# Kernel tuning notes

Measured on AMD Instinct MI355X. Metric: run time of the kernel, lower is better.

The kernel has to match this reference:

```python
import jax, jax.numpy as jnp
import numpy as np

EPS = 1e-12  # matches torch F.normalize default eps in spectral_norm


def _l2norm(v):
    return v / jnp.maximum(jnp.linalg.norm(v), EPS)


def _spectral_norm(W, u):
    # One power-iteration step (torch spectral_norm training behavior).
    # u, v are treated as constants w.r.t. gradients.
    v = jax.lax.stop_gradient(_l2norm(W.T @ u))
    u2 = jax.lax.stop_gradient(_l2norm(W @ v))
    sigma = jnp.einsum('o,oi,i->', u2, W, v)
    return W / sigma


def setup_inputs() -> dict:
    key = jax.random.key(0)
    ks = jax.random.split(key, 8)
    B, C, N = 8, 512, 2048
    d = C // 8
    return {
        'x':  jax.random.normal(ks[0], (B, C, N), dtype=jnp.float32),
        'Wq': jax.random.normal(ks[1], (d, C), dtype=jnp.float32) * (1.0 / np.sqrt(C)),
        'Wk': jax.random.normal(ks[2], (d, C), dtype=jnp.float32) * (1.0 / np.sqrt(C)),
        'Wv': jax.random.normal(ks[3], (C, C), dtype=jnp.float32) * (1.0 / np.sqrt(C)),
        'uq': jax.random.normal(ks[4], (d,), dtype=jnp.float32),
        'uk': jax.random.normal(ks[5], (d,), dtype=jnp.float32),
        'uv': jax.random.normal(ks[6], (C,), dtype=jnp.float32),
        'gamma': jax.random.normal(ks[7], (1,), dtype=jnp.float32) * 0.1,
    }


def reference(x, Wq, Wk, Wv, uq, uk, uv, gamma):
    # x: [B, C, N]
    f = jnp.einsum('oi,bin->bon', _spectral_norm(Wq, uq), x)  # [B, C/8, N]
    g = jnp.einsum('oi,bin->bon', _spectral_norm(Wk, uk), x)  # [B, C/8, N]
    h = jnp.einsum('oi,bin->bon', _spectral_norm(Wv, uv), x)  # [B, C, N]
    scores = jnp.einsum('bdn,bdm->bnm', f, g)                 # f^T g: [B, N, N]
    beta = jax.nn.softmax(scores, axis=1)                      # softmax over dim=1
    o = gamma[0] * jnp.einsum('bcn,bnm->bcm', h, beta) + x    # [B, C, N]
    return o
```

## Files before the change

kernel.cpp:

```cpp
#include <hip/hip_runtime.h>
#include <hip/hip_bf16.h>
#include <math.h>

#define B_ 8
#define C_ 512
#define N_ 2048
#define D_ 64
#define O_ 640

typedef __bf16 bf16x8 __attribute__((ext_vector_type(8)));
typedef float f32x4 __attribute__((ext_vector_type(4)));
typedef unsigned short ushort8_t __attribute__((ext_vector_type(8)));
typedef unsigned short ushort4_t __attribute__((ext_vector_type(4)));

__device__ __forceinline__ unsigned short f2bf(float f) {
    unsigned int u = __builtin_bit_cast(unsigned int, f);
    u += 0x7fffu + ((u >> 16) & 1u);
    return (unsigned short)(u >> 16);
}

__device__ __forceinline__ float fastexp(float x) {
    return exp2f(x * 1.44269504088896340736f);
}

union FragU { ushort8_t u; bf16x8 b; };

__device__ __forceinline__ bf16x8 ldfrag(const unsigned short* p) {
    FragU t; t.u = *(const ushort8_t*)p; return t.b;
}

__device__ __forceinline__ void gload_lds16(const unsigned short* g, unsigned short* l) {
    __builtin_amdgcn_global_load_lds((const __attribute__((address_space(1))) void*)g,
                                     (__attribute__((address_space(3))) void*)l,
                                     16, 0, 0);
}

__global__ __launch_bounds__(512) void k_colvec(const float* __restrict__ Wq,
                                                const float* __restrict__ Wk,
                                                const float* __restrict__ Wv,
                                                const float* __restrict__ uq,
                                                const float* __restrict__ uk,
                                                const float* __restrict__ uv,
                                                float* __restrict__ tpart) {
    int which = blockIdx.y, oq = blockIdx.x;
    const float* W; const float* u; int R;
    if (which == 0)      { W = Wq; u = uq; R = 64;  }
    else if (which == 1) { W = Wk; u = uk; R = 64;  }
    else                 { W = Wv; u = uv; R = 512; }
    int chunk = R >> 2;
    int i = threadIdx.x;
    float s = 0.f;
    int o0 = oq * chunk, o1 = o0 + chunk;
    for (int o = o0; o < o1; ++o) s += W[(size_t)o * 512 + i] * u[o];
    tpart[((which << 2) + oq) * 512 + i] = s;
}

__global__ __launch_bounds__(512) void k_trow(const float* __restrict__ tpart,
                                              float* __restrict__ tvec,
                                              float* __restrict__ t2) {
    int which = blockIdx.x, i = threadIdx.x;
    const float* tp = tpart + (which << 2) * 512;
    float s = tp[i] + tp[512 + i] + tp[1024 + i] + tp[1536 + i];
    tvec[which * 512 + i] = s;
    __shared__ float red[512];
    red[i] = s * s; __syncthreads();
    for (int st = 256; st > 0; st >>= 1) { if (i < st) red[i] += red[i + st]; __syncthreads(); }
    if (i == 0) t2[which] = red[0];
}

__global__ __launch_bounds__(256) void k_rowvec(const float* __restrict__ Wq,
                                                const float* __restrict__ Wk,
                                                const float* __restrict__ Wv,
                                                const float* __restrict__ tvec,
                                                float* __restrict__ wpart) {
    int which = blockIdx.y;
    const float* W; int R;
    if (which == 0)      { W = Wq; R = 64;  }
    else if (which == 1) { W = Wk; R = 64;  }
    else                 { W = Wv; R = 512; }
    int tid = threadIdx.x, lane = tid & 63, wv = tid >> 6;
    int row = blockIdx.x * 4 + wv;
    float ps = 0.f;
    if (row < R) {
        const float4* wr_ = (const float4*)(W + (size_t)row * 512);
        const float4* tv = (const float4*)(tvec + which * 512);
        float4 a0 = wr_[lane * 2], a1 = wr_[lane * 2 + 1];
        float4 b0 = tv[lane * 2], b1 = tv[lane * 2 + 1];
        float s = a0.x * b0.x + a0.y * b0.y + a0.z * b0.z + a0.w * b0.w
                + a1.x * b1.x + a1.y * b1.y + a1.z * b1.z + a1.w * b1.w;
        #pragma unroll
        for (int off = 1; off < 64; off <<= 1) s += __shfl_xor(s, off, 64);
        ps = s * s;
    }
    __shared__ float red[4];
    if (lane == 0) red[wv] = ps;
    __syncthreads();
    if (tid == 0) wpart[which * 128 + blockIdx.x] = red[0] + red[1] + red[2] + red[3];
}

__global__ __launch_bounds__(128) void k_scale(const float* __restrict__ wpart,
                                               const float* __restrict__ t2,
                                               float* __restrict__ scales) {
    int which = blockIdx.x, tid = threadIdx.x;
    float s = wpart[which * 128 + tid];
    #pragma unroll
    for (int off = 1; off < 64; off <<= 1) s += __shfl_xor(s, off, 64);
    __shared__ float r2[2];
    if ((tid & 63) == 0) r2[tid >> 6] = s;
    __syncthreads();
    if (tid == 0) scales[which] = sqrtf(t2[which] / fmaxf(r2[0] + r2[1], 1e-24f));
}

__global__ __launch_bounds__(256) void k_wconv(const float* __restrict__ Wq,
                                               const float* __restrict__ Wk,
                                               const float* __restrict__ Wv,
                                               const float* __restrict__ scales,
                                               unsigned short* __restrict__ Wb) {
    int gid = blockIdx.x * 256 + threadIdx.x;
    int e0 = gid * 8;
    int o = e0 >> 9, i = e0 & 511;
    const float* src; float sc;
    if (o < 64)       { src = Wq + (size_t)o * 512;         sc = scales[0]; }
    else if (o < 128) { src = Wk + (size_t)(o - 64) * 512;  sc = scales[1]; }
    else              { src = Wv + (size_t)(o - 128) * 512; sc = scales[2]; }
    float4 v0 = *(const float4*)(src + i), v1 = *(const float4*)(src + i + 4);
    ushort8_t u;
    u[0] = f2bf(v0.x * sc); u[1] = f2bf(v0.y * sc); u[2] = f2bf(v0.z * sc); u[3] = f2bf(v0.w * sc);
    u[4] = f2bf(v1.x * sc); u[5] = f2bf(v1.y * sc); u[6] = f2bf(v1.z * sc); u[7] = f2bf(v1.w * sc);
    *(ushort8_t*)&Wb[(size_t)o * 512 + i] = u;
}

__global__ __launch_bounds__(256) void k_transpose(const float* __restrict__ x,
                                                   unsigned short* __restrict__ xT) {
    __shared__ float tile[64][33];
    int b = blockIdx.z;
    int n0 = blockIdx.x * 32, c0 = blockIdx.y * 64;
    int tx = threadIdx.x, ty = threadIdx.y;
    #pragma unroll
    for (int k = 0; k < 8; ++k) {
        int c = ty + k * 8;
        tile[c][tx] = x[((size_t)b * C_ + c0 + c) * N_ + n0 + tx];
    }
    __syncthreads();
    #pragma unroll
    for (int k = 0; k < 4; ++k) {
        int n = ty + k * 8;
        unsigned int p = (unsigned int)f2bf(tile[tx * 2][n]) |
                         ((unsigned int)f2bf(tile[tx * 2 + 1][n]) << 16);
        *(unsigned int*)&xT[((size_t)b * N_ + n0 + n) * C_ + c0 + tx * 2] = p;
    }
}

__global__ __launch_bounds__(256) void k_proj(const unsigned short* __restrict__ xT,
                                              const unsigned short* __restrict__ Wb,
                                              unsigned short* __restrict__ fT,
                                              unsigned short* __restrict__ gT,
                                              unsigned short* __restrict__ hb) {
    int b = blockIdx.z, n0 = blockIdx.y * 128, o0 = blockIdx.x * 128;
    int tid = threadIdx.x, lane = tid & 63, w = tid >> 6;
    int wr = w >> 1, wc = w & 1;
    __shared__ __align__(16) unsigned short Sh[16384];
    unsigned short* As = Sh;
    unsigned short* Bs = Sh + 8192;
    f32x4 zero = {0.f, 0.f, 0.f, 0.f};
    f32x4 acc[4][4];
    #pragma unroll
    for (int i = 0; i < 4; ++i)
        #pragma unroll
        for (int j = 0; j < 4; ++j) acc[i][j] = zero;
    int r8 = lane >> 3, s = lane & 7;
    int scol = (s ^ r8) * 8;

    for (int kt = 0; kt < 8; ++kt) {
        #pragma unroll
        for (int q = 0; q < 4; ++q) {
            int chunk = w * 4 + q;
            int row = chunk * 8 + r8;
            gload_lds16(xT + ((size_t)b * N_ + n0 + row) * C_ + kt * 64 + scol, &As[chunk * 512]);
            gload_lds16(Wb + (size_t)(o0 + row) * C_ + kt * 64 + scol, &Bs[chunk * 512]);
        }
        __syncthreads();
        int kg = lane >> 4, r16 = lane & 15;
        #pragma unroll
        for (int kk = 0; kk < 2; ++kk) {
            int sw = kk * 4 + kg;
            bf16x8 af[4];
            #pragma unroll
            for (int i = 0; i < 4; ++i) {
                int row = wr * 64 + i * 16 + r16;
                af[i] = ldfrag(&As[row * 64 + (sw ^ (row & 7)) * 8]);
            }
            #pragma unroll
            for (int j = 0; j < 4; ++j) {
                int row = wc * 64 + j * 16 + r16;
                bf16x8 bv = ldfrag(&Bs[row * 64 + (sw ^ (row & 7)) * 8]);
                #pragma unroll
                for (int i = 0; i < 4; ++i)
                    acc[i][j] = __builtin_amdgcn_mfma_f32_16x16x32_bf16(af[i], bv, acc[i][j], 0, 0, 0);
            }
        }
        __syncthreads();
    }

    unsigned short* St = Sh;
    if (o0 == 0) {
        #pragma unroll
        for (int p = 0; p < 2; ++p) {
            if (wc == p) {
                #pragma unroll
                for (int i = 0; i < 4; ++i)
                    #pragma unroll
                    for (int j = 0; j < 4; ++j)
                        #pragma unroll
                        for (int r = 0; r < 4; ++r)
                            St[(wr * 64 + i * 16 + (lane >> 4) * 4 + r) * 72 + j * 16 + (lane & 15)] = f2bf(acc[i][j][r]);
            }
            __syncthreads();
            unsigned short* dst = p == 0 ? fT : gT;
            #pragma unroll
            for (int it = 0; it < 4; ++it) {
                int row = it * 32 + (tid >> 3);
                *(ushort8_t*)&dst[((size_t)b * N_ + n0 + row) * D_ + (tid & 7) * 8] =
                    *(ushort8_t*)&St[row * 72 + (tid & 7) * 8];
            }
            __syncthreads();
        }
    } else {
        int ho0 = o0 - 128;
        #pragma unroll
        for (int p = 0; p < 2; ++p) {
            if (wc == p) {
                #pragma unroll
                for (int i = 0; i < 4; ++i)
                    #pragma unroll
                    for (int j = 0; j < 4; ++j)
                        #pragma unroll
                        for (int r = 0; r < 4; ++r)
                            St[(j * 16 + (lane & 15)) * 136 + wr * 64 + i * 16 + (lane >> 4) * 4 + r] = f2bf(acc[i][j][r]);
            }
            __syncthreads();
            #pragma unroll
            for (int it = 0; it < 4; ++it) {
                int row = it * 16 + (tid >> 4);
                *(ushort8_t*)&hb[((size_t)b * C_ + ho0 + p * 64 + row) * N_ + n0 + (tid & 15) * 8] =
                    *(ushort8_t*)&St[row * 136 + (tid & 15) * 8];
            }
            __syncthreads();
        }
    }
}

__global__ __launch_bounds__(256) void k_stats(const unsigned short* __restrict__ fT,
                                               const unsigned short* __restrict__ gT,
                                               float* __restrict__ colmax,
                                               float* __restrict__ colsinv) {
    int b = blockIdx.y, m0 = blockIdx.x * 16;
    int tid = threadIdx.x, lane = tid & 63, w = tid >> 6;
    int mcol = m0 + (lane & 15);
    const unsigned short* gbase = gT + ((size_t)b * N_ + mcol) * D_ + (lane >> 4) * 8;
    bf16x8 g0 = ldfrag(gbase);
    bf16x8 g1 = ldfrag(gbase + 32);

    float mx = -1e30f, sm = 0.f;
    for (int nt = w * 32; nt < w * 32 + 32; ++nt) {
        const unsigned short* abase = fT + ((size_t)b * N_ + nt * 16 + (lane & 15)) * D_ + (lane >> 4) * 8;
        f32x4 s = {0.f, 0.f, 0.f, 0.f};
        s = __builtin_amdgcn_mfma_f32_16x16x32_bf16(ldfrag(abase), g0, s, 0, 0, 0);
        s = __builtin_amdgcn_mfma_f32_16x16x32_bf16(ldfrag(abase + 32), g1, s, 0, 0, 0);
        float tm = fmaxf(fmaxf(s[0], s[1]), fmaxf(s[2], s[3]));
        float nm = fmaxf(mx, tm);
        float c = fastexp(mx - nm);
        sm = sm * c + fastexp(s[0] - nm) + fastexp(s[1] - nm) + fastexp(s[2] - nm) + fastexp(s[3] - nm);
        mx = nm;
    }
    #pragma unroll
    for (int off = 16; off < 64; off <<= 1) {
        float omx = __shfl_xor(mx, off, 64);
        float osm = __shfl_xor(sm, off, 64);
        float nm = fmaxf(mx, omx);
        sm = sm * fastexp(mx - nm) + osm * fastexp(omx - nm);
        mx = nm;
    }
    __shared__ float lmx[4][16], lsm[4][16];
    if ((lane >> 4) == 0) { lmx[w][lane & 15] = mx; lsm[w][lane & 15] = sm; }
    __syncthreads();
    if (tid < 16) {
        float M = lmx[0][tid], S = lsm[0][tid];
        #pragma unroll
        for (int q = 1; q < 4; ++q) {
            float om = lmx[q][tid], os = lsm[q][tid];
            float nm = fmaxf(M, om);
            S = S * fastexp(M - nm) + os * fastexp(om - nm);
            M = nm;
        }
        colmax[(size_t)b * N_ + m0 + tid] = M;
        colsinv[(size_t)b * N_ + m0 + tid] = 1.0f / S;
    }
}

__global__ __launch_bounds__(256) void k_beta(const unsigned short* __restrict__ fT,
                                              const unsigned short* __restrict__ gT,
                                              const float* __restrict__ colmax,
                                              const float* __restrict__ colsinv,
                                              unsigned short* __restrict__ betaT) {
    int b = blockIdx.z, n0 = blockIdx.y * 64, m0 = blockIdx.x * 64;
    int tid = threadIdx.x, lane = tid & 63, w = tid >> 6;
    __shared__ __align__(16) unsigned short St[64 * 72];
    const unsigned short* abase = fT + ((size_t)b * N_ + n0 + w * 16 + (lane & 15)) * D_ + (lane >> 4) * 8;
    bf16x8 a0 = ldfrag(abase);
    bf16x8 a1 = ldfrag(abase + 32);
    const int SP = 72;
    #pragma unroll
    for (int j = 0; j < 4; ++j) {
        int m = m0 + j * 16 + (lane & 15);
        const unsigned short* gbase = gT + ((size_t)b * N_ + m) * D_ + (lane >> 4) * 8;
        f32x4 s = {0.f, 0.f, 0.f, 0.f};
        s = __builtin_amdgcn_mfma_f32_16x16x32_bf16(a0, ldfrag(gbase), s, 0, 0, 0);
        s = __builtin_amdgcn_mfma_f32_16x16x32_bf16(a1, ldfrag(gbase + 32), s, 0, 0, 0);
        float mxv = colmax[(size_t)b * N_ + m];
        float siv = colsinv[(size_t)b * N_ + m];
        #pragma unroll
        for (int r = 0; r < 4; ++r)
            St[(j * 16 + (lane & 15)) * SP + w * 16 + (lane >> 4) * 4 + r] = f2bf(fastexp(s[r] - mxv) * siv);
    }
    __syncthreads();
    int rr = tid >> 3, cp = (tid & 7) * 8;
    #pragma unroll
    for (int it = 0; it < 2; ++it) {
        int m = rr + it * 32;
        *(ushort8_t*)&betaT[((size_t)b * N_ + m0 + m) * N_ + n0 + cp] = *(ushort8_t*)&St[m * SP + cp];
    }
}

__global__ __launch_bounds__(256) void k_pv(const unsigned short* __restrict__ betaT,
                                            const unsigned short* __restrict__ hb,
                                            const float* __restrict__ x,
                                            const float* __restrict__ gamma,
                                            float* __restrict__ out) {
    int b = blockIdx.z, m0 = blockIdx.x * 64, c0 = blockIdx.y * 128;
    int tid = threadIdx.x, lane = tid & 63, w = tid >> 6;
    int wm = w >> 1, wc = w & 1;
    __shared__ __align__(16) unsigned short As[64 * 64];
    __shared__ __align__(16) unsigned short Bs[128 * 64];
    f32x4 zero = {0.f, 0.f, 0.f, 0.f};
    f32x4 acc[2][4];
    #pragma unroll
    for (int i = 0; i < 2; ++i)
        #pragma unroll
        for (int j = 0; j < 4; ++j) acc[i][j] = zero;
    int srow = lane >> 3;
    int scb = ((lane & 7) ^ srow) * 8;

    for (int kt = 0; kt < N_ / 64; ++kt) {
        #pragma unroll
        for (int q = 0; q < 2; ++q) {
            int chunk = w * 2 + q;
            int row = chunk * 8 + srow;
            gload_lds16(betaT + ((size_t)b * N_ + m0 + row) * N_ + kt * 64 + scb, &As[chunk * 512]);
        }
        #pragma unroll
        for (int q = 0; q < 4; ++q) {
            int chunk = w * 4 + q;
            int row = chunk * 8 + srow;
            gload_lds16(hb + ((size_t)b * C_ + c0 + row) * N_ + kt * 64 + scb, &Bs[chunk * 512]);
        }
        __syncthreads();
        #pragma unroll
        for (int kk = 0; kk < 2; ++kk) {
            int colg = kk * 32 + (lane >> 4) * 8;
            bf16x8 af[2];
            #pragma unroll
            for (int i = 0; i < 2; ++i) {
                int ar = wm * 32 + i * 16 + (lane & 15);
                af[i] = ldfrag(&As[ar * 64 + (colg ^ ((ar & 7) << 3))]);
            }
            #pragma unroll
            for (int j = 0; j < 4; ++j) {
                int br = wc * 64 + j * 16 + (lane & 15);
                bf16x8 bv = ldfrag(&Bs[br * 64 + (colg ^ ((br & 7) << 3))]);
                #pragma unroll
                for (int i = 0; i < 2; ++i)
                    acc[i][j] = __builtin_amdgcn_mfma_f32_16x16x32_bf16(af[i], bv, acc[i][j], 0, 0, 0);
            }
        }
        __syncthreads();
    }

    float gv = gamma[0];
    #pragma unroll
    for (int i = 0; i < 2; ++i) {
        int mb = m0 + wm * 32 + i * 16 + (lane >> 4) * 4;
        #pragma unroll
        for (int j = 0; j < 4; ++j) {
            int c = c0 + wc * 64 + j * 16 + (lane & 15);
            size_t base = ((size_t)b * C_ + c) * N_ + mb;
            float4 xv = *(const float4*)(x + base);
            float4 ov;
            ov.x = gv * acc[i][j][0] + xv.x;
            ov.y = gv * acc[i][j][1] + xv.y;
            ov.z = gv * acc[i][j][2] + xv.z;
            ov.w = gv * acc[i][j][3] + xv.w;
            *(float4*)(out + base) = ov;
        }
    }
}

extern "C" void kernel_launch(void* const* d_in, const int* in_sizes, int n_in,
                              void* d_out, int out_size, void* d_ws, size_t ws_size,
                              hipStream_t stream) {
    const float* x     = (const float*)d_in[0];
    const float* Wq    = (const float*)d_in[1];
    const float* Wk    = (const float*)d_in[2];
    const float* Wv    = (const float*)d_in[3];
    const float* uq    = (const float*)d_in[4];
    const float* uk    = (const float*)d_in[5];
    const float* uv    = (const float*)d_in[6];
    const float* gamma = (const float*)d_in[7];
    float* out = (float*)d_out;

    char* wsb = (char*)d_ws;
    float* scales         = (float*)wsb;
    unsigned short* xT    = (unsigned short*)(wsb + 256);
    unsigned short* fT    = xT + (size_t)B_ * N_ * C_;
    unsigned short* gT    = fT + (size_t)B_ * N_ * D_;
    unsigned short* hb    = gT + (size_t)B_ * N_ * D_;
    unsigned short* betaT = hb + (size_t)B_ * C_ * N_;
    float* colmax         = (float*)(betaT + (size_t)B_ * N_ * N_);
    float* colsinv        = colmax + (size_t)B_ * N_;
    float* tpart          = colsinv + (size_t)B_ * N_;
    float* tvec           = tpart + 3 * 4 * 512;
    float* t2             = tvec + 3 * 512;
    float* wpart          = t2 + 16;
    unsigned short* Wb    = (unsigned short*)(wpart + 3 * 128);

    k_colvec<<<dim3(4, 3), 512, 0, stream>>>(Wq, Wk, Wv, uq, uk, uv, tpart);
    k_trow<<<3, 512, 0, stream>>>(tpart, tvec, t2);
    k_rowvec<<<dim3(128, 3), 256, 0, stream>>>(Wq, Wk, Wv, tvec, wpart);
    k_scale<<<3, 128, 0, stream>>>(wpart, t2, scales);
    k_wconv<<<O_ * C_ / (256 * 8), 256, 0, stream>>>(Wq, Wk, Wv, scales, Wb);
    k_transpose<<<dim3(N_ / 32, C_ / 64, B_), dim3(32, 8), 0, stream>>>(x, xT);
    k_proj<<<dim3(O_ / 128, N_ / 128, B_), 256, 0, stream>>>(xT, Wb, fT, gT, hb);
    k_stats<<<dim3(N_ / 16, B_), 256, 0, stream>>>(fT, gT, colmax, colsinv);
    k_beta<<<dim3(N_ / 64, N_ / 64, B_), 256, 0, stream>>>(fT, gT, colmax, colsinv, betaT);
    k_pv<<<dim3(N_ / 64, C_ / 128, B_), 256, 0, stream>>>(betaT, hb, x, gamma, out);
}
```

Measured before the change: 200.2 us.

## Fuse beta computation into PV GEMM, removing materialized attention matrix

Replaces the separate k_beta kernel, which wrote the full bf16 attention matrix to global memory, and the k_pv kernel that read it back, with one fused kernel. Each tile of scores is recomputed from f and g fragments in LDS, normalised with the precomputed column stats, and fed straight into the MFMA accumulation against h. This removes the 64MB global write and read of betaT. It also uses 512-thread blocks with 128x256 output tiles, double-buffered LDS loads and a block-index swizzle. The cost is that each of the two channel halves recomputes the scores, plus higher register and LDS pressure.

Result: faster. 186.5 us, median of 3 (-6.9%).

```diff
diff --git a/kernel.cpp b/kernel.cpp
--- a/kernel.cpp
+++ b/kernel.cpp
@@ -298,102 +298,127 @@
     }
 }
 
-__global__ __launch_bounds__(256) void k_beta(const unsigned short* __restrict__ fT,
-                                              const unsigned short* __restrict__ gT,
-                                              const float* __restrict__ colmax,
-                                              const float* __restrict__ colsinv,
-                                              unsigned short* __restrict__ betaT) {
-    int b = blockIdx.z, n0 = blockIdx.y * 64, m0 = blockIdx.x * 64;
-    int tid = threadIdx.x, lane = tid & 63, w = tid >> 6;
-    __shared__ __align__(16) unsigned short St[64 * 72];
-    const unsigned short* abase = fT + ((size_t)b * N_ + n0 + w * 16 + (lane & 15)) * D_ + (lane >> 4) * 8;
-    bf16x8 a0 = ldfrag(abase);
-    bf16x8 a1 = ldfrag(abase + 32);
-    const int SP = 72;
-    #pragma unroll
-    for (int j = 0; j < 4; ++j) {
-        int m = m0 + j * 16 + (lane & 15);
-        const unsigned short* gbase = gT + ((size_t)b * N_ + m) * D_ + (lane >> 4) * 8;
-        f32x4 s = {0.f, 0.f, 0.f, 0.f};
-        s = __builtin_amdgcn_mfma_f32_16x16x32_bf16(a0, ldfrag(gbase), s, 0, 0, 0);
-        s = __builtin_amdgcn_mfma_f32_16x16x32_bf16(a1, ldfrag(gbase + 32), s, 0, 0, 0);
-        float mxv = colmax[(size_t)b * N_ + m];
-        float siv = colsinv[(size_t)b * N_ + m];
-        #pragma unroll
-        for (int r = 0; r < 4; ++r)
-            St[(j * 16 + (lane & 15)) * SP + w * 16 + (lane >> 4) * 4 + r] = f2bf(fastexp(s[r] - mxv) * siv);
-    }
-    __syncthreads();
-    int rr = tid >> 3, cp = (tid & 7) * 8;
-    #pragma unroll
-    for (int it = 0; it < 2; ++it) {
-        int m = rr + it * 32;
-        *(ushort8_t*)&betaT[((size_t)b * N_ + m0 + m) * N_ + n0 + cp] = *(ushort8_t*)&St[m * SP + cp];
-    }
-}
-
-__global__ __launch_bounds__(256) void k_pv(const unsigned short* __restrict__ betaT,
+__global__ __launch_bounds__(512) void k_av(const unsigned short* __restrict__ fT,
+                                            const unsigned short* __restrict__ gT,
                                             const unsigned short* __restrict__ hb,
+                                            const float* __restrict__ colmax,
+                                            const float* __restrict__ colsinv,
                                             const float* __restrict__ x,
                                             const float* __restrict__ gamma,
                                             float* __restrict__ out) {
-    int b = blockIdx.z, m0 = blockIdx.x * 64, c0 = blockIdx.y * 128;
+    __shared__ __align__(16) unsigned short FT[2][4096];
+    __shared__ __align__(16) unsigned short HB[2][16384];
+    __shared__ __align__(16) unsigned short BS[8192];
+
+    int bid = blockIdx.x;
+    int xg = bid & 7, sidx = bid >> 3;
+    int bc = xg + 8 * (sidx >> 4);
+    int mi = sidx & 15;
+    int b = bc >> 1, ch = bc & 1;
+    int m0 = mi * 128, c0 = ch * 256;
+
     int tid = threadIdx.x, lane = tid & 63, w = tid >> 6;
-    int wm = w >> 1, wc = w & 1;
-    __shared__ __align__(16) unsigned short As[64 * 64];
-    __shared__ __align__(16) unsigned short Bs[128 * 64];
+    int nw = w & 3, mh = w >> 2;
+    int l15 = lane & 15, lq = lane >> 4;
+    int r8 = lane >> 3, sl = lane & 7;
+    int scol = (sl ^ r8) * 8;
+
+    bf16x8 gf[4][2];
+    float mx_[4], siv_[4];
+    #pragma unroll
+    for (int j = 0; j < 4; ++j) {
+        int m = m0 + mh * 64 + j * 16 + l15;
+        #pragma unroll
+        for (int kd = 0; kd < 2; ++kd)
+            gf[j][kd] = ldfrag(gT + ((size_t)b * N_ + m) * D_ + kd * 32 + lq * 8);
+        mx_[j] = colmax[(size_t)b * N_ + m];
+        siv_[j] = colsinv[(size_t)b * N_ + m];
+    }
+
     f32x4 zero = {0.f, 0.f, 0.f, 0.f};
-    f32x4 acc[2][4];
-    #pragma unroll
-    for (int i = 0; i < 2; ++i)
+    f32x4 acc[4][4];
+    #pragma unroll
+    for (int i = 0; i < 4; ++i)
         #pragma unroll
         for (int j = 0; j < 4; ++j) acc[i][j] = zero;
-    int srow = lane >> 3;
-    int scb = ((lane & 7) ^ srow) * 8;
-
+
+    const unsigned short* fbase = fT + ((size_t)b * N_) * D_;
+    const unsigned short* hbase = hb + ((size_t)b * C_ + c0) * N_;
+
+    {
+        int frow = w * 8 + r8;
+        gload_lds16(fbase + (size_t)frow * D_ + scol, &FT[0][w * 512]);
+        #pragma unroll
+        for (int q = 0; q < 4; ++q) {
+            int ci = w * 4 + q;
+            int crow = ci * 8 + r8;
+            gload_lds16(hbase + (size_t)crow * N_ + scol, &HB[0][ci * 512]);
+        }
+    }
+
+    int buf = 0;
     for (int kt = 0; kt < N_ / 64; ++kt) {
-        #pragma unroll
-        for (int q = 0; q < 2; ++q) {
-            int chunk = w * 2 + q;
-            int row = chunk * 8 + srow;
-            gload_lds16(betaT + ((size_t)b * N_ + m0 + row) * N_ + kt * 64 + scb, &As[chunk * 512]);
-        }
-        #pragma unroll
-        for (int q = 0; q < 4; ++q) {
-            int chunk = w * 4 + q;
-            int row = chunk * 8 + srow;
-            gload_lds16(hb + ((size_t)b * C_ + c0 + row) * N_ + kt * 64 + scb, &Bs[chunk * 512]);
-        }
         __syncthreads();
+
+        int arow = nw * 16 + l15;
+        bf16x8 af0 = ldfrag(&FT[buf][arow * 64 + ((lq ^ (arow & 7)) * 8)]);
+        bf16x8 af1 = ldfrag(&FT[buf][arow * 64 + (((4 + lq) ^ (arow & 7)) * 8)]);
+        #pragma unroll
+        for (int j = 0; j < 4; ++j) {
+            f32x4 sv = zero;
+            sv = __builtin_amdgcn_mfma_f32_16x16x32_bf16(af0, gf[j][0], sv, 0, 0, 0);
+            sv = __builtin_amdgcn_mfma_f32_16x16x32_bf16(af1, gf[j][1], sv, 0, 0, 0);
+            int mrel = mh * 64 + j * 16 + l15;
+            ushort4_t pk;
+            #pragma unroll
+            for (int r = 0; r < 4; ++r)
+                pk[r] = f2bf(fastexp(sv[r] - mx_[j]) * siv_[j]);
+            int nt = nw * 16 + lq * 4;
+            *(ushort4_t*)&BS[mrel * 64 + (((nt >> 3) ^ (mrel & 7)) * 8) + (nt & 7)] = pk;
+        }
+        __syncthreads();
+
+        if (kt + 1 < N_ / 64) {
+            int nb = buf ^ 1;
+            int frow = w * 8 + r8;
+            gload_lds16(fbase + ((size_t)(kt + 1) * 64 + frow) * D_ + scol, &FT[nb][w * 512]);
+            #pragma unroll
+            for (int q = 0; q < 4; ++q) {
+                int ci = w * 4 + q;
+                int crow = ci * 8 + r8;
+                gload_lds16(hbase + (size_t)crow * N_ + (kt + 1) * 64 + scol, &HB[nb][ci * 512]);
+            }
+        }
+
         #pragma unroll
         for (int kk = 0; kk < 2; ++kk) {
-            int colg = kk * 32 + (lane >> 4) * 8;
-            bf16x8 af[2];
-            #pragma unroll
-            for (int i = 0; i < 2; ++i) {
-                int ar = wm * 32 + i * 16 + (lane & 15);
-                af[i] = ldfrag(&As[ar * 64 + (colg ^ ((ar & 7) << 3))]);
+            int ng = kk * 4 + lq;
+            bf16x8 pa[4];
+            #pragma unroll
+            for (int i = 0; i < 4; ++i) {
+                int mr = mh * 64 + i * 16 + l15;
+                pa[i] = ldfrag(&BS[mr * 64 + ((ng ^ (mr & 7)) * 8)]);
             }
             #pragma unroll
             for (int j = 0; j < 4; ++j) {
-                int br = wc * 64 + j * 16 + (lane & 15);
-                bf16x8 bv = ldfrag(&Bs[br * 64 + (colg ^ ((br & 7) << 3))]);
+                int cr = nw * 64 + j * 16 + l15;
+                bf16x8 hv = ldfrag(&HB[buf][cr * 64 + ((ng ^ (cr & 7)) * 8)]);
                 #pragma unroll
-                for (int i = 0; i < 2; ++i)
-                    acc[i][j] = __builtin_amdgcn_mfma_f32_16x16x32_bf16(af[i], bv, acc[i][j], 0, 0, 0);
-            }
-        }
-        __syncthreads();
+                for (int i = 0; i < 4; ++i)
+                    acc[i][j] = __builtin_amdgcn_mfma_f32_16x16x32_bf16(pa[i], hv, acc[i][j], 0, 0, 0);
+            }
+        }
+        buf ^= 1;
     }
 
     float gv = gamma[0];
     #pragma unroll
-    for (int i = 0; i < 2; ++i) {
-        int mb = m0 + wm * 32 + i * 16 + (lane >> 4) * 4;
+    for (int i = 0; i < 4; ++i) {
+        int mabs = m0 + mh * 64 + i * 16 + lq * 4;
         #pragma unroll
         for (int j = 0; j < 4; ++j) {
-            int c = c0 + wc * 64 + j * 16 + (lane & 15);
-            size_t base = ((size_t)b * C_ + c) * N_ + mb;
+            int cabs = c0 + nw * 64 + j * 16 + l15;
+            size_t base = ((size_t)b * C_ + cabs) * N_ + mabs;
             float4 xv = *(const float4*)(x + base);
             float4 ov;
             ov.x = gv * acc[i][j][0] + xv.x;
@@ -424,8 +449,7 @@
     unsigned short* fT    = xT + (size_t)B_ * N_ * C_;
     unsigned short* gT    = fT + (size_t)B_ * N_ * D_;
     unsigned short* hb    = gT + (size_t)B_ * N_ * D_;
-    unsigned short* betaT = hb + (size_t)B_ * C_ * N_;
-    float* colmax         = (float*)(betaT + (size_t)B_ * N_ * N_);
+    float* colmax         = (float*)(hb + (size_t)B_ * C_ * N_);
     float* colsinv        = colmax + (size_t)B_ * N_;
     float* tpart          = colsinv + (size_t)B_ * N_;
     float* tvec           = tpart + 3 * 4 * 512;
@@ -441,6 +465,5 @@
     k_transpose<<<dim3(N_ / 32, C_ / 64, B_), dim3(32, 8), 0, stream>>>(x, xT);
     k_proj<<<dim3(O_ / 128, N_ / 128, B_), 256, 0, stream>>>(xT, Wb, fT, gT, hb);
     k_stats<<<dim3(N_ / 16, B_), 256, 0, stream>>>(fT, gT, colmax, colsinv);
-    k_beta<<<dim3(N_ / 64, N_ / 64, B_), 256, 0, stream>>>(fT, gT, colmax, colsinv, betaT);
-    k_pv<<<dim3(N_ / 64, C_ / 128, B_), 256, 0, stream>>>(betaT, hb, x, gamma, out);
-}
+    k_av<<<256, 512, 0, stream>>>(fT, gT, hb, colmax, colsinv, x, gamma, out);
+}
```

## Double-buffer LDS tiles in projection and PV GEMMs to overlap loads with MFMA

Applied to the files above, without the earlier changes.

Converts the k_proj and k_pv main loops to a two-stage LDS ping-pong. The next K-tile is issued via direct global-to-LDS loads before the MFMA work on the current tile, with one barrier per iteration instead of two. Wave priority is raised around the MFMA section. The aim is to hide global memory latency behind compute, at the cost of doubled shared memory per block, which may reduce occupancy.

Result: slower. 211.1 us (+5.4%).

```diff
diff --git a/kernel.cpp b/kernel.cpp
--- a/kernel.cpp
+++ b/kernel.cpp
@@ -156,22 +156,23 @@
                                               unsigned short* __restrict__ fT,
                                               unsigned short* __restrict__ gT,
                                               unsigned short* __restrict__ hb) {
+    const int NT = 8;
     int b = blockIdx.z, n0 = blockIdx.y * 128, o0 = blockIdx.x * 128;
     int tid = threadIdx.x, lane = tid & 63, w = tid >> 6;
     int wr = w >> 1, wc = w & 1;
-    __shared__ __align__(16) unsigned short Sh[16384];
-    unsigned short* As = Sh;
-    unsigned short* Bs = Sh + 8192;
+    __shared__ __align__(16) unsigned short Sh[32768];
     f32x4 zero = {0.f, 0.f, 0.f, 0.f};
     f32x4 acc[4][4];
     #pragma unroll
     for (int i = 0; i < 4; ++i)
         #pragma unroll
         for (int j = 0; j < 4; ++j) acc[i][j] = zero;
-    int r8 = lane >> 3, s = lane & 7;
-    int scol = (s ^ r8) * 8;
-
-    for (int kt = 0; kt < 8; ++kt) {
+    int r8 = lane >> 3, sl = lane & 7;
+    int scol = (sl ^ r8) * 8;
+
+    auto STAGE = [&](int kt, int p) {
+        unsigned short* As = Sh + p * 8192;
+        unsigned short* Bs = Sh + 16384 + p * 8192;
         #pragma unroll
         for (int q = 0; q < 4; ++q) {
             int chunk = w * 4 + q;
@@ -179,8 +180,23 @@
             gload_lds16(xT + ((size_t)b * N_ + n0 + row) * C_ + kt * 64 + scol, &As[chunk * 512]);
             gload_lds16(Wb + (size_t)(o0 + row) * C_ + kt * 64 + scol, &Bs[chunk * 512]);
         }
-        __syncthreads();
-        int kg = lane >> 4, r16 = lane & 15;
+    };
+
+    STAGE(0, 0);
+    asm volatile("s_waitcnt vmcnt(0)" ::: "memory");
+    __builtin_amdgcn_sched_barrier(0);
+    __builtin_amdgcn_s_barrier();
+    __builtin_amdgcn_sched_barrier(0);
+
+    int kg = lane >> 4, r16 = lane & 15;
+    #pragma unroll 1
+    for (int kt = 0; kt < NT; ++kt) {
+        int p = kt & 1;
+        if (kt + 1 < NT) STAGE(kt + 1, p ^ 1);
+        __builtin_amdgcn_sched_barrier(0);
+        const unsigned short* As = Sh + p * 8192;
+        const unsigned short* Bs = Sh + 16384 + p * 8192;
+        __builtin_amdgcn_s_setprio(1);
         #pragma unroll
         for (int kk = 0; kk < 2; ++kk) {
             int sw = kk * 4 + kg;
@@ -199,8 +215,15 @@
                     acc[i][j] = __builtin_amdgcn_mfma_f32_16x16x32_bf16(af[i], bv, acc[i][j], 0, 0, 0);
             }
         }
-        __syncthreads();
-    }
+        __builtin_amdgcn_s_setprio(0);
+        if (kt + 1 < NT) {
+            asm volatile("s_waitcnt vmcnt(0)" ::: "memory");
+            __builtin_amdgcn_sched_barrier(0);
+            __builtin_amdgcn_s_barrier();
+            __builtin_amdgcn_sched_barrier(0);
+        }
+    }
+    __syncthreads();
 
     unsigned short* St = Sh;
     if (o0 == 0) {
@@ -310,11 +333,12 @@
     bf16x8 a0 = ldfrag(abase);
     bf16x8 a1 = ldfrag(abase + 32);
     const int SP = 72;
+    f32x4 zero = {0.f, 0.f, 0.f, 0.f};
     #pragma unroll
     for (int j = 0; j < 4; ++j) {
         int m = m0 + j * 16 + (lane & 15);
         const unsigned short* gbase = gT + ((size_t)b * N_ + m) * D_ + (lane >> 4) * 8;
-        f32x4 s = {0.f, 0.f, 0.f, 0.f};
+        f32x4 s = zero;
         s = __builtin_amdgcn_mfma_f32_16x16x32_bf16(a0, ldfrag(gbase), s, 0, 0, 0);
         s = __builtin_amdgcn_mfma_f32_16x16x32_bf16(a1, ldfrag(gbase + 32), s, 0, 0, 0);
         float mxv = colmax[(size_t)b * N_ + m];
@@ -337,11 +361,12 @@
                                             const float* __restrict__ x,
                                             const float* __restrict__ gamma,
                                             float* __restrict__ out) {
+    const int NT = N_ / 64;
     int b = blockIdx.z, m0 = blockIdx.x * 64, c0 = blockIdx.y * 128;
     int tid = threadIdx.x, lane = tid & 63, w = tid >> 6;
     int wm = w >> 1, wc = w & 1;
-    __shared__ __align__(16) unsigned short As[64 * 64];
-    __shared__ __align__(16) unsigned short Bs[128 * 64];
+    __shared__ __align__(16) unsigned short As[2][4096];
+    __shared__ __align__(16) unsigned short Bs[2][8192];
     f32x4 zero = {0.f, 0.f, 0.f, 0.f};
     f32x4 acc[2][4];
     #pragma unroll
@@ -351,20 +376,33 @@
     int srow = lane >> 3;
     int scb = ((lane & 7) ^ srow) * 8;
 
-    for (int kt = 0; kt < N_ / 64; ++kt) {
+    auto STAGE = [&](int kt, int p) {
         #pragma unroll
         for (int q = 0; q < 2; ++q) {
             int chunk = w * 2 + q;
             int row = chunk * 8 + srow;
-            gload_lds16(betaT + ((size_t)b * N_ + m0 + row) * N_ + kt * 64 + scb, &As[chunk * 512]);
+            gload_lds16(betaT + ((size_t)b * N_ + m0 + row) * N_ + kt * 64 + scb, &As[p][chunk * 512]);
         }
         #pragma unroll
         for (int q = 0; q < 4; ++q) {
             int chunk = w * 4 + q;
             int row = chunk * 8 + srow;
-            gload_lds16(hb + ((size_t)b * C_ + c0 + row) * N_ + kt * 64 + scb, &Bs[chunk * 512]);
-        }
-        __syncthreads();
+            gload_lds16(hb + ((size_t)b * C_ + c0 + row) * N_ + kt * 64 + scb, &Bs[p][chunk * 512]);
+        }
+    };
+
+    STAGE(0, 0);
+    asm volatile("s_waitcnt vmcnt(0)" ::: "memory");
+    __builtin_amdgcn_sched_barrier(0);
+    __builtin_amdgcn_s_barrier();
+    __builtin_amdgcn_sched_barrier(0);
+
+    #pragma unroll 1
+    for (int kt = 0; kt < NT; ++kt) {
+        int p = kt & 1;
+        if (kt + 1 < NT) STAGE(kt + 1, p ^ 1);
+        __builtin_amdgcn_sched_barrier(0);
+        __builtin_amdgcn_s_setprio(1);
         #pragma unroll
         for (int kk = 0; kk < 2; ++kk) {
             int colg = kk * 32 + (lane >> 4) * 8;
@@ -372,18 +410,24 @@
             #pragma unroll
             for (int i = 0; i < 2; ++i) {
                 int ar = wm * 32 + i * 16 + (lane & 15);
-                af[i] = ldfrag(&As[ar * 64 + (colg ^ ((ar & 7) << 3))]);
+                af[i] = ldfrag(&As[p][ar * 64 + (colg ^ ((ar & 7) << 3))]);
             }
             #pragma unroll
             for (int j = 0; j < 4; ++j) {
                 int br = wc * 64 + j * 16 + (lane & 15);
-                bf16x8 bv = ldfrag(&Bs[br * 64 + (colg ^ ((br & 7) << 3))]);
+                bf16x8 bv = ldfrag(&Bs[p][br * 64 + (colg ^ ((br & 7) << 3))]);
                 #pragma unroll
                 for (int i = 0; i < 2; ++i)
                     acc[i][j] = __builtin_amdgcn_mfma_f32_16x16x32_bf16(af[i], bv, acc[i][j], 0, 0, 0);
             }
         }
-        __syncthreads();
+        __builtin_amdgcn_s_setprio(0);
+        if (kt + 1 < NT) {
+            asm volatile("s_waitcnt vmcnt(0)" ::: "memory");
+            __builtin_amdgcn_sched_barrier(0);
+            __builtin_amdgcn_s_barrier();
+            __builtin_amdgcn_sched_barrier(0);
+        }
     }
 
     float gv = gamma[0];
```
